# Kernel tuning notes

Hardware: AMD Instinct MI355X
Metric: run time of the kernel (lower is better)

The kernel has to match this reference:

```python
import jax, jax.numpy as jnp
import numpy as np

D_MODEL = 1024
NUM_HEADS = 16
D_K = D_MODEL // NUM_HEADS
B, S = 2, 2048
NEG = -1e9


def setup_inputs() -> dict:
    key = jax.random.key(0)
    ks = jax.random.split(key, 12)
    scale = 1.0 / np.sqrt(D_MODEL)
    inp = {
        'q': jax.random.normal(ks[0], (B, S, D_MODEL), jnp.float32),
        'k': jax.random.normal(ks[1], (B, S, D_MODEL), jnp.float32),
        'v': jax.random.normal(ks[2], (B, S, D_MODEL), jnp.float32),
        'mask': jax.random.randint(ks[3], (1, 1, S, S), 0, 2, jnp.int32),
        'wq_w': jax.random.normal(ks[4], (D_MODEL, D_MODEL), jnp.float32) * scale,
        'wq_b': jnp.zeros((D_MODEL,), jnp.float32),
        'wk_w': jax.random.normal(ks[5], (D_MODEL, D_MODEL), jnp.float32) * scale,
        'wk_b': jnp.zeros((D_MODEL,), jnp.float32),
        'wv_w': jax.random.normal(ks[6], (D_MODEL, D_MODEL), jnp.float32) * scale,
        'wv_b': jnp.zeros((D_MODEL,), jnp.float32),
        'wo_w': jax.random.normal(ks[7], (D_MODEL, D_MODEL), jnp.float32) * scale,
        'wo_b': jnp.zeros((D_MODEL,), jnp.float32),
    }
    return inp


def _split_heads(x):
    # [B,S,D] -> [B,H,S,d_k]
    b, s, _ = x.shape
    return x.reshape(b, s, NUM_HEADS, D_K).transpose(0, 2, 1, 3)


def reference(q, k, v, mask, wq_w, wq_b, wk_w, wk_b, wv_w, wv_b, wo_w, wo_b):
    # torch Linear: y = x @ W.T + b
    qh = _split_heads(q @ wq_w.T + wq_b)
    kh = _split_heads(k @ wk_w.T + wk_b)
    vh = _split_heads(v @ wv_w.T + wv_b)
    scores = jnp.einsum('bhqd,bhkd->bhqk', qh, kh) / jnp.sqrt(jnp.float32(D_K))
    scores = jnp.where(mask == 0, jnp.float32(NEG), scores)
    attn = jax.nn.softmax(scores, axis=-1)  # dropout p=0 (eval): no-op
    x = jnp.einsum('bhqk,bhkd->bhqd', attn, vh)
    x = x.transpose(0, 2, 1, 3).reshape(q.shape[0], q.shape[1], D_MODEL)
    return x @ wo_w.T + wo_b
```

## Files before the change

kernel.cpp:

```cpp
#include <hip/hip_runtime.h>
#include <hip/hip_bf16.h>
#include <stdint.h>

#define S_LEN  2048
#define DMODEL 1024
#define NHEADS 16
#define DKH    64
#define KDIM   1024

typedef __bf16 bf16x8 __attribute__((ext_vector_type(8)));
typedef float  floatx4 __attribute__((ext_vector_type(4)));
typedef unsigned short ushort8v __attribute__((ext_vector_type(8)));

__device__ inline void gll16(const __bf16* g, const __bf16* l) {
    __builtin_amdgcn_global_load_lds(
        (const __attribute__((address_space(1))) void*)g,
        (__attribute__((address_space(3))) void*)l, 16, 0, 0);
}

__global__ __launch_bounds__(256) void convert_all_kernel(
    const float* __restrict__ q, const float* __restrict__ k, const float* __restrict__ v,
    const float* __restrict__ wq, const float* __restrict__ wk, const float* __restrict__ wv,
    const float* __restrict__ wo, __bf16* __restrict__ out) {
    const size_t i8 = ((size_t)blockIdx.x * 256 + threadIdx.x) * 8;
    const float* src;
    if (i8 < 4194304u)        src = q  + i8;
    else if (i8 < 8388608u)   src = k  + (i8 - 4194304u);
    else if (i8 < 12582912u)  src = v  + (i8 - 8388608u);
    else if (i8 < 13631488u)  src = wq + (i8 - 12582912u);
    else if (i8 < 14680064u)  src = wk + (i8 - 13631488u);
    else if (i8 < 15728640u)  src = wv + (i8 - 14680064u);
    else                      src = wo + (i8 - 15728640u);
    floatx4 a = *(const floatx4*)src;
    floatx4 b = *(const floatx4*)(src + 4);
    bf16x8 r;
#pragma unroll
    for (int i = 0; i < 4; ++i) { r[i] = (__bf16)a[i]; r[i + 4] = (__bf16)b[i]; }
    *(bf16x8*)(out + i8) = r;
}

__global__ __launch_bounds__(256) void maskpack_kernel(const int* __restrict__ M,
                                                       uint64_t* __restrict__ P) {
    const size_t i = (size_t)blockIdx.x * 256 + threadIdx.x;
    uint64_t bits = __ballot(M[i] != 0);
    if ((threadIdx.x & 63) == 0) P[i >> 6] = bits;
}

__global__ __launch_bounds__(256) void qkv_gemm(
    const __bf16* __restrict__ qb, const __bf16* __restrict__ kb, const __bf16* __restrict__ vb,
    const __bf16* __restrict__ wqw, const __bf16* __restrict__ wkw, const __bf16* __restrict__ wvw,
    const float* __restrict__ biasq, const float* __restrict__ biask, const float* __restrict__ biasv,
    __bf16* __restrict__ qh, __bf16* __restrict__ kh, __bf16* __restrict__ vt) {
    __shared__ __align__(16) __bf16 As[2 * 128 * 32];
    __shared__ __align__(16) __bf16 Bs[2 * 128 * 32];

    const int lane = threadIdx.x & 63;
    const int wave = threadIdx.x >> 6;
    const int quad = lane >> 4;
    const int l15  = lane & 15;

    const int bid = blockIdx.x;
    const int job = bid >> 8;
    const int tt  = bid & 255;
    const __bf16* A; const __bf16* Bm; const float* bias; __bf16* C;
    int bx, by, MODE;
    if (job == 0)      { A = qb;  Bm = wqw; bias = biasq; C = qh; bx = tt & 7;  by = tt >> 3; MODE = 0; }
    else if (job == 1) { A = kb;  Bm = wkw; bias = biask; C = kh; bx = tt & 7;  by = tt >> 3; MODE = 0; }
    else               { A = wvw; Bm = vb;  bias = biasv; C = vt; bx = tt & 31; by = tt >> 5; MODE = 1; }

    const int m_t = by * 128, n_t = bx * 128;
    const int m0w = (wave >> 1) * 64, n0w = (wave & 1) * 64;

    const int sp = wave >> 1;
    const int sr = (wave & 1) * 64;
    const int lrow = lane >> 2;
    const int scol = ((lane & 3) ^ (lrow & 3)) * 8;

    floatx4 acc[4][4];
#pragma unroll
    for (int i = 0; i < 4; ++i)
#pragma unroll
        for (int j = 0; j < 4; ++j)
            acc[i][j] = (floatx4){0.f, 0.f, 0.f, 0.f};

    for (int kk = 0; kk < KDIM; kk += 64) {
#pragma unroll
        for (int c = 0; c < 4; ++c) {
            const int row = sr + c * 16 + lrow;
            gll16(A + (size_t)(m_t + row) * KDIM + kk + sp * 32 + scol,
                  As + (sp * 128 + sr + c * 16) * 32);
            gll16(Bm + (size_t)(n_t + row) * KDIM + kk + sp * 32 + scol,
                  Bs + (sp * 128 + sr + c * 16) * 32);
        }
        __syncthreads();
        const int cq = (quad ^ (l15 & 3)) * 8;
#pragma unroll
        for (int p = 0; p < 2; ++p) {
            bf16x8 af[4], bfr[4];
#pragma unroll
            for (int i = 0; i < 4; ++i)
                af[i] = *(const bf16x8*)(As + (p * 128 + m0w + i * 16 + l15) * 32 + cq);
#pragma unroll
            for (int j = 0; j < 4; ++j)
                bfr[j] = *(const bf16x8*)(Bs + (p * 128 + n0w + j * 16 + l15) * 32 + cq);
#pragma unroll
            for (int i = 0; i < 4; ++i)
#pragma unroll
                for (int j = 0; j < 4; ++j)
                    acc[i][j] = __builtin_amdgcn_mfma_f32_16x16x32_bf16(af[i], bfr[j], acc[i][j], 0, 0, 0);
        }
        __syncthreads();
    }

#pragma unroll
    for (int j = 0; j < 4; ++j) {
        const int n = n_t + n0w + j * 16 + l15;
        float bn = (MODE == 1) ? 0.f : bias[n];
#pragma unroll
        for (int i = 0; i < 4; ++i) {
#pragma unroll
            for (int r = 0; r < 4; ++r) {
                const int m = m_t + m0w + i * 16 + quad * 4 + r;
                float bv = (MODE == 1) ? bias[m] : bn;
                float v = acc[i][j][r] + bv;
                size_t off;
                if (MODE == 0) {
                    off = ((size_t)((m >> 11) * 16 + (n >> 6)) * 2048 + (m & 2047)) * 64 + (n & 63);
                } else {
                    off = ((size_t)((n >> 11) * 16 + (m >> 6)) * 64 + (m & 63)) * 2048 + (n & 2047);
                }
                C[off] = (__bf16)v;
            }
        }
    }
}

__global__ __launch_bounds__(256) void gemm_out(const __bf16* __restrict__ A,
                                                const __bf16* __restrict__ Bm,
                                                const float* __restrict__ bias,
                                                float* __restrict__ C) {
    __shared__ __align__(16) __bf16 As[2 * 128 * 32];
    __shared__ __align__(16) __bf16 Bs[2 * 64 * 32];

    const int lane = threadIdx.x & 63;
    const int wave = threadIdx.x >> 6;
    const int quad = lane >> 4;
    const int l15  = lane & 15;
    const int m_t = blockIdx.y * 128, n_t = blockIdx.x * 64;
    const int m0w = (wave >> 1) * 64, n0w = (wave & 1) * 32;

    const int lrow = lane >> 2;
    const int scol = ((lane & 3) ^ (lrow & 3)) * 8;

    floatx4 acc[4][2];
#pragma unroll
    for (int i = 0; i < 4; ++i)
#pragma unroll
        for (int j = 0; j < 2; ++j)
            acc[i][j] = (floatx4){0.f, 0.f, 0.f, 0.f};

    for (int kk = 0; kk < KDIM; kk += 64) {
#pragma unroll
        for (int u = 0; u < 6; ++u) {
            const int pi = wave * 6 + u;
            if (pi < 16) {
                const int panel = pi >> 3, rb = pi & 7;
                gll16(A + (size_t)(m_t + rb * 16 + lrow) * KDIM + kk + panel * 32 + scol,
                      As + (panel * 128 + rb * 16) * 32);
            } else {
                const int qi = pi - 16, panel = qi >> 2, rb = qi & 3;
                gll16(Bm + (size_t)(n_t + rb * 16 + lrow) * KDIM + kk + panel * 32 + scol,
                      Bs + (panel * 64 + rb * 16) * 32);
            }
        }
        __syncthreads();
        const int cq = (quad ^ (l15 & 3)) * 8;
#pragma unroll
        for (int p = 0; p < 2; ++p) {
            bf16x8 af[4], bfr[2];
#pragma unroll
            for (int i = 0; i < 4; ++i)
                af[i] = *(const bf16x8*)(As + (p * 128 + m0w + i * 16 + l15) * 32 + cq);
#pragma unroll
            for (int j = 0; j < 2; ++j)
                bfr[j] = *(const bf16x8*)(Bs + (p * 64 + n0w + j * 16 + l15) * 32 + cq);
#pragma unroll
            for (int i = 0; i < 4; ++i)
#pragma unroll
                for (int j = 0; j < 2; ++j)
                    acc[i][j] = __builtin_amdgcn_mfma_f32_16x16x32_bf16(af[i], bfr[j], acc[i][j], 0, 0, 0);
        }
        __syncthreads();
    }

#pragma unroll
    for (int j = 0; j < 2; ++j) {
        const int n = n_t + n0w + j * 16 + l15;
        const float bn = bias[n];
#pragma unroll
        for (int i = 0; i < 4; ++i)
#pragma unroll
            for (int r = 0; r < 4; ++r) {
                const int m = m_t + m0w + i * 16 + quad * 4 + r;
                C[(size_t)m * 1024 + n] = acc[i][j][r] + bn;
            }
    }
}

__global__ __launch_bounds__(256) void attn_kernel(const __bf16* __restrict__ Qh,
                                                   const __bf16* __restrict__ Kh,
                                                   const __bf16* __restrict__ Vt,
                                                   const uint64_t* __restrict__ PM,
                                                   __bf16* __restrict__ X) {
    __shared__ __align__(16) __bf16 Ks[2][4096];
    __shared__ __align__(16) __bf16 Vs[2][4096];

    const int lane = threadIdx.x & 63;
    const int wave = threadIdx.x >> 6;
    const int quad = lane >> 4;
    const int l15  = lane & 15;
    const int l7   = l15 & 7;

    const int bid  = blockIdx.x;
    const int xcd  = bid & 7;
    const int slot = bid >> 3;
    const int grp  = xcd * 4 + (slot >> 4);
    const int qt   = slot & 15;
    const int b = grp >> 4, h = grp & 15;
    const int q0 = qt * 128 + wave * 32;

    const __bf16* Qb = Qh + (size_t)(b * NHEADS + h) * S_LEN * DKH;
    const __bf16* Kb = Kh + (size_t)(b * NHEADS + h) * S_LEN * DKH;
    const __bf16* Vb = Vt + (size_t)(b * NHEADS + h) * DKH * S_LEN;
    const uint64_t* pr0 = PM + (size_t)(q0 + l15) * (S_LEN / 64);
    const uint64_t* pr1 = PM + (size_t)(q0 + 16 + l15) * (S_LEN / 64);

    const float cs = 0.18033688011112042f;
    const float MB = 4.0f;

    size_t offK[2], offV[2];
#pragma unroll
    for (int i = 0; i < 2; ++i) {
        const int s = wave * 128 + i * 64 + lane;
        const int r = s >> 3, cp = s & 7, c = cp ^ (r & 7);
        const int kr = (r >> 5) * 32 + ((r >> 4) & 1) * 4 + ((r >> 2) & 3) * 8 + (r & 3);
        offK[i] = (size_t)kr * DKH + c * 8;
        offV[i] = (size_t)r * S_LEN + c * 8;
    }

    bf16x8 qf[2][2];
#pragma unroll
    for (int s = 0; s < 2; ++s)
#pragma unroll
        for (int c = 0; c < 2; ++c)
            qf[s][c] = *(const bf16x8*)(Qb + (size_t)(q0 + s * 16 + l15) * DKH + c * 32 + quad * 8);

    floatx4 o[2][4];
#pragma unroll
    for (int s = 0; s < 2; ++s)
#pragma unroll
        for (int f = 0; f < 4; ++f) o[s][f] = (floatx4){0.f, 0.f, 0.f, 0.f};
    float lsum[2] = {0.f, 0.f};

    auto stage = [&](int p, int key0) {
#pragma unroll
        for (int i = 0; i < 2; ++i) {
            gll16(Kb + (size_t)key0 * DKH + offK[i], &Ks[p][(wave * 128 + i * 64) * 8]);
            gll16(Vb + key0 + offV[i],               &Vs[p][(wave * 128 + i * 64) * 8]);
        }
    };

    stage(0, 0);
    for (int kt = 0; kt < 32; ++kt) {
        const int p = kt & 1;
        __syncthreads();
        if (kt < 31) stage(p ^ 1, (kt + 1) * 64);

        const uint64_t mw0 = pr0[kt];
        const uint64_t mw1 = pr1[kt];

        bf16x8 kf[4][2];
#pragma unroll
        for (int t = 0; t < 4; ++t)
#pragma unroll
            for (int hh = 0; hh < 2; ++hh) {
                const int cp = ((hh * 4 + quad) ^ l7) * 8;
                kf[t][hh] = *(const bf16x8*)&Ks[p][(t * 16 + l15) * 64 + cp];
            }

        floatx4 st[2][4];
#pragma unroll
        for (int s = 0; s < 2; ++s)
#pragma unroll
            for (int t = 0; t < 4; ++t) {
                floatx4 z = (floatx4){0.f, 0.f, 0.f, 0.f};
                z = __builtin_amdgcn_mfma_f32_16x16x32_bf16(kf[t][0], qf[s][0], z, 0, 0, 0);
                z = __builtin_amdgcn_mfma_f32_16x16x32_bf16(kf[t][1], qf[s][1], z, 0, 0, 0);
                st[s][t] = z;
            }

        bf16x8 pw[2][2];
#pragma unroll
        for (int s = 0; s < 2; ++s) {
            const uint64_t mw = s ? mw1 : mw0;
#pragma unroll
            for (int w = 0; w < 2; ++w) {
                bf16x8 pb;
#pragma unroll
                for (int half = 0; half < 2; ++half) {
                    const int t = w * 2 + half;
                    const int sh = w * 32 + half * 4 + quad * 8;
#pragma unroll
                    for (int r = 0; r < 4; ++r) {
                        float e = exp2f(fmaf(st[s][t][r], cs, -MB));
                        e = ((mw >> (sh + r)) & 1u) ? e : 0.f;
                        lsum[s] += e;
                        pb[half * 4 + r] = (__bf16)e;
                    }
                }
                pw[s][w] = pb;
            }
        }

#pragma unroll
        for (int w = 0; w < 2; ++w) {
            const int cp = ((w * 4 + quad) ^ l7) * 8;
#pragma unroll
            for (int f = 0; f < 4; ++f) {
                bf16x8 vf = *(const bf16x8*)&Vs[p][(f * 16 + l15) * 64 + cp];
                o[0][f] = __builtin_amdgcn_mfma_f32_16x16x32_bf16(vf, pw[0][w], o[0][f], 0, 0, 0);
                o[1][f] = __builtin_amdgcn_mfma_f32_16x16x32_bf16(vf, pw[1][w], o[1][f], 0, 0, 0);
            }
        }
    }

    float inv[2];
#pragma unroll
    for (int s = 0; s < 2; ++s) {
        float t = lsum[s];
        t += __shfl_xor(t, 16);
        t += __shfl_xor(t, 32);
        inv[s] = (t > 0.f) ? (1.f / t) : 0.f;
    }

    __syncthreads();
    unsigned short* xw = (unsigned short*)&Ks[0][0] + wave * (16 * 80);
#pragma unroll
    for (int s = 0; s < 2; ++s) {
#pragma unroll
        for (int f = 0; f < 4; ++f)
#pragma unroll
            for (int r = 0; r < 4; ++r) {
                __bf16 bv = (__bf16)(o[s][f][r] * inv[s]);
                xw[l15 * 80 + f * 16 + quad * 4 + r] = __builtin_bit_cast(unsigned short, bv);
            }
#pragma unroll
        for (int it = 0; it < 2; ++it) {
            const int ql = it * 8 + (lane >> 3);
            const int dseg = (lane & 7) * 8;
            ushort8v vv = *(const ushort8v*)&xw[ql * 80 + dseg];
            unsigned short* dst = (unsigned short*)X +
                (size_t)(b * S_LEN + q0 + s * 16 + ql) * DMODEL + h * DKH + dseg;
            *(ushort8v*)dst = vv;
        }
    }
}

extern "C" void kernel_launch(void* const* d_in, const int* in_sizes, int n_in,
                              void* d_out, int out_size, void* d_ws, size_t ws_size,
                              hipStream_t stream) {
    const float* q   = (const float*)d_in[0];
    const float* k   = (const float*)d_in[1];
    const float* v   = (const float*)d_in[2];
    const int*   msk = (const int*)d_in[3];
    const float* wq  = (const float*)d_in[4];
    const float* wqb = (const float*)d_in[5];
    const float* wk  = (const float*)d_in[6];
    const float* wkb = (const float*)d_in[7];
    const float* wv  = (const float*)d_in[8];
    const float* wvb = (const float*)d_in[9];
    const float* wo  = (const float*)d_in[10];
    const float* wob = (const float*)d_in[11];

    char* ws = (char*)d_ws;
    __bf16*   qh   = (__bf16*)(ws);
    __bf16*   kh   = (__bf16*)(ws + 8388608);
    __bf16*   vt   = (__bf16*)(ws + 16777216);
    uint64_t* pm   = (uint64_t*)(ws + 25165824);
    __bf16*   cb   = (__bf16*)(ws + 25690112);
    __bf16*   qb   = cb;
    __bf16*   kb   = cb + 4194304;
    __bf16*   vb   = cb + 8388608;
    __bf16*   wqbf = cb + 12582912;
    __bf16*   wkbf = cb + 13631488;
    __bf16*   wvbf = cb + 14680064;
    __bf16*   wobf = cb + 15728640;
    __bf16*   xa   = qb;

    convert_all_kernel<<<8192, 256, 0, stream>>>(q, k, v, wq, wk, wv, wo, cb);
    maskpack_kernel<<<16384, 256, 0, stream>>>(msk, pm);
    qkv_gemm<<<768, 256, 0, stream>>>(qb, kb, vb, wqbf, wkbf, wvbf, wqb, wkb, wvb, qh, kh, vt);
    attn_kernel<<<512, 256, 0, stream>>>(qh, kh, vt, pm, xa);
    gemm_out<<<dim3(16, 32), 256, 0, stream>>>(xa, wobf, wob, (float*)d_out);
}
```

Measured before the change: 296.4 us.

## Halve attention query tile per wave, double grid, compute row sums via MFMA

The attention kernel now gives each wave 16 query rows instead of 32, so each block covers 64 queries and the grid doubles to 1024 blocks with a launch-bounds occupancy hint of 4. The softmax denominator is accumulated with an extra MFMA against a ones vector instead of per-lane adds and shuffles. The code also uses a hardware exp2 builtin, applies the mask with a sign-bit AND, and prefetches the mask word one iteration ahead. The aim is more waves in flight and fewer VALU instructions, at the cost of reloading K/V tiles from LDS for half as many queries per block, which roughly doubles K/V traffic.

```diff
diff --git a/kernel.cpp b/kernel.cpp
--- a/kernel.cpp
+++ b/kernel.cpp
@@ -16,6 +16,14 @@
     __builtin_amdgcn_global_load_lds(
         (const __attribute__((address_space(1))) void*)g,
         (__attribute__((address_space(3))) void*)l, 16, 0, 0);
+}
+
+__device__ inline float fast_exp2(float x) {
+#if __has_builtin(__builtin_amdgcn_exp2f)
+    return __builtin_amdgcn_exp2f(x);
+#else
+    return exp2f(x);
+#endif
 }
 
 __global__ __launch_bounds__(256) void convert_all_kernel(
@@ -207,11 +215,11 @@
     }
 }
 
-__global__ __launch_bounds__(256) void attn_kernel(const __bf16* __restrict__ Qh,
-                                                   const __bf16* __restrict__ Kh,
-                                                   const __bf16* __restrict__ Vt,
-                                                   const uint64_t* __restrict__ PM,
-                                                   __bf16* __restrict__ X) {
+__global__ __launch_bounds__(256, 4) void attn_kernel(const __bf16* __restrict__ Qh,
+                                                      const __bf16* __restrict__ Kh,
+                                                      const __bf16* __restrict__ Vt,
+                                                      const uint64_t* __restrict__ PM,
+                                                      __bf16* __restrict__ X) {
     __shared__ __align__(16) __bf16 Ks[2][4096];
     __shared__ __align__(16) __bf16 Vs[2][4096];
 
@@ -224,16 +232,15 @@
     const int bid  = blockIdx.x;
     const int xcd  = bid & 7;
     const int slot = bid >> 3;
-    const int grp  = xcd * 4 + (slot >> 4);
-    const int qt   = slot & 15;
+    const int grp  = xcd * 4 + (slot >> 5);
+    const int qt   = slot & 31;
     const int b = grp >> 4, h = grp & 15;
-    const int q0 = qt * 128 + wave * 32;
+    const int q0 = qt * 64 + wave * 16;
 
     const __bf16* Qb = Qh + (size_t)(b * NHEADS + h) * S_LEN * DKH;
     const __bf16* Kb = Kh + (size_t)(b * NHEADS + h) * S_LEN * DKH;
     const __bf16* Vb = Vt + (size_t)(b * NHEADS + h) * DKH * S_LEN;
-    const uint64_t* pr0 = PM + (size_t)(q0 + l15) * (S_LEN / 64);
-    const uint64_t* pr1 = PM + (size_t)(q0 + 16 + l15) * (S_LEN / 64);
+    const uint64_t* pr = PM + (size_t)(q0 + l15) * (S_LEN / 64);
 
     const float cs = 0.18033688011112042f;
     const float MB = 4.0f;
@@ -248,19 +255,19 @@
         offV[i] = (size_t)r * S_LEN + c * 8;
     }
 
-    bf16x8 qf[2][2];
-#pragma unroll
-    for (int s = 0; s < 2; ++s)
-#pragma unroll
-        for (int c = 0; c < 2; ++c)
-            qf[s][c] = *(const bf16x8*)(Qb + (size_t)(q0 + s * 16 + l15) * DKH + c * 32 + quad * 8);
-
-    floatx4 o[2][4];
-#pragma unroll
-    for (int s = 0; s < 2; ++s)
-#pragma unroll
-        for (int f = 0; f < 4; ++f) o[s][f] = (floatx4){0.f, 0.f, 0.f, 0.f};
-    float lsum[2] = {0.f, 0.f};
+    bf16x8 qf[2];
+#pragma unroll
+    for (int c = 0; c < 2; ++c)
+        qf[c] = *(const bf16x8*)(Qb + (size_t)(q0 + l15) * DKH + c * 32 + quad * 8);
+
+    bf16x8 ones;
+#pragma unroll
+    for (int i = 0; i < 8; ++i) ones[i] = (__bf16)1.0f;
+
+    floatx4 o[4], osum;
+#pragma unroll
+    for (int f = 0; f < 4; ++f) o[f] = (floatx4){0.f, 0.f, 0.f, 0.f};
+    osum = (floatx4){0.f, 0.f, 0.f, 0.f};
 
     auto stage = [&](int p, int key0) {
 #pragma unroll
@@ -271,13 +278,13 @@
     };
 
     stage(0, 0);
+    uint2 mwc = *(const uint2*)(pr);
     for (int kt = 0; kt < 32; ++kt) {
         const int p = kt & 1;
         __syncthreads();
         if (kt < 31) stage(p ^ 1, (kt + 1) * 64);
-
-        const uint64_t mw0 = pr0[kt];
-        const uint64_t mw1 = pr1[kt];
+        const uint2 mw = mwc;
+        if (kt < 31) mwc = *(const uint2*)(pr + kt + 1);
 
         bf16x8 kf[4][2];
 #pragma unroll
@@ -288,38 +295,33 @@
                 kf[t][hh] = *(const bf16x8*)&Ks[p][(t * 16 + l15) * 64 + cp];
             }
 
-        floatx4 st[2][4];
-#pragma unroll
-        for (int s = 0; s < 2; ++s)
-#pragma unroll
-            for (int t = 0; t < 4; ++t) {
-                floatx4 z = (floatx4){0.f, 0.f, 0.f, 0.f};
-                z = __builtin_amdgcn_mfma_f32_16x16x32_bf16(kf[t][0], qf[s][0], z, 0, 0, 0);
-                z = __builtin_amdgcn_mfma_f32_16x16x32_bf16(kf[t][1], qf[s][1], z, 0, 0, 0);
-                st[s][t] = z;
-            }
-
-        bf16x8 pw[2][2];
-#pragma unroll
-        for (int s = 0; s < 2; ++s) {
-            const uint64_t mw = s ? mw1 : mw0;
-#pragma unroll
-            for (int w = 0; w < 2; ++w) {
-                bf16x8 pb;
-#pragma unroll
-                for (int half = 0; half < 2; ++half) {
-                    const int t = w * 2 + half;
-                    const int sh = w * 32 + half * 4 + quad * 8;
-#pragma unroll
-                    for (int r = 0; r < 4; ++r) {
-                        float e = exp2f(fmaf(st[s][t][r], cs, -MB));
-                        e = ((mw >> (sh + r)) & 1u) ? e : 0.f;
-                        lsum[s] += e;
-                        pb[half * 4 + r] = (__bf16)e;
-                    }
+        floatx4 st[4];
+#pragma unroll
+        for (int t = 0; t < 4; ++t) {
+            floatx4 z = (floatx4){0.f, 0.f, 0.f, 0.f};
+            z = __builtin_amdgcn_mfma_f32_16x16x32_bf16(kf[t][0], qf[0], z, 0, 0, 0);
+            z = __builtin_amdgcn_mfma_f32_16x16x32_bf16(kf[t][1], qf[1], z, 0, 0, 0);
+            st[t] = z;
+        }
+
+        bf16x8 pw[2];
+#pragma unroll
+        for (int w = 0; w < 2; ++w) {
+            const uint32_t byte = (w ? mw.y : mw.x) >> (quad * 8);
+            bf16x8 pb;
+#pragma unroll
+            for (int half = 0; half < 2; ++half) {
+                const int t = w * 2 + half;
+#pragma unroll
+                for (int r = 0; r < 4; ++r) {
+                    const int idx = half * 4 + r;
+                    float e = fast_exp2(fmaf(st[t][r], cs, -MB));
+                    const int sgn = ((int)(byte << (31 - idx))) >> 31;
+                    e = __builtin_bit_cast(float, __builtin_bit_cast(int, e) & sgn);
+                    pb[half * 4 + r] = (__bf16)e;
                 }
-                pw[s][w] = pb;
-            }
+            }
+            pw[w] = pb;
         }
 
 #pragma unroll
@@ -328,41 +330,32 @@
 #pragma unroll
             for (int f = 0; f < 4; ++f) {
                 bf16x8 vf = *(const bf16x8*)&Vs[p][(f * 16 + l15) * 64 + cp];
-                o[0][f] = __builtin_amdgcn_mfma_f32_16x16x32_bf16(vf, pw[0][w], o[0][f], 0, 0, 0);
-                o[1][f] = __builtin_amdgcn_mfma_f32_16x16x32_bf16(vf, pw[1][w], o[1][f], 0, 0, 0);
-            }
-        }
-    }
-
-    float inv[2];
-#pragma unroll
-    for (int s = 0; s < 2; ++s) {
-        float t = lsum[s];
-        t += __shfl_xor(t, 16);
-        t += __shfl_xor(t, 32);
-        inv[s] = (t > 0.f) ? (1.f / t) : 0.f;
-    }
+                o[f] = __builtin_amdgcn_mfma_f32_16x16x32_bf16(vf, pw[w], o[f], 0, 0, 0);
+            }
+            osum = __builtin_amdgcn_mfma_f32_16x16x32_bf16(ones, pw[w], osum, 0, 0, 0);
+        }
+    }
+
+    const float lsum = osum[0];
+    const float inv = (lsum > 0.f) ? (1.f / lsum) : 0.f;
 
     __syncthreads();
     unsigned short* xw = (unsigned short*)&Ks[0][0] + wave * (16 * 80);
 #pragma unroll
-    for (int s = 0; s < 2; ++s) {
-#pragma unroll
-        for (int f = 0; f < 4; ++f)
-#pragma unroll
-            for (int r = 0; r < 4; ++r) {
-                __bf16 bv = (__bf16)(o[s][f][r] * inv[s]);
-                xw[l15 * 80 + f * 16 + quad * 4 + r] = __builtin_bit_cast(unsigned short, bv);
-            }
-#pragma unroll
-        for (int it = 0; it < 2; ++it) {
-            const int ql = it * 8 + (lane >> 3);
-            const int dseg = (lane & 7) * 8;
-            ushort8v vv = *(const ushort8v*)&xw[ql * 80 + dseg];
-            unsigned short* dst = (unsigned short*)X +
-                (size_t)(b * S_LEN + q0 + s * 16 + ql) * DMODEL + h * DKH + dseg;
-            *(ushort8v*)dst = vv;
-        }
+    for (int f = 0; f < 4; ++f)
+#pragma unroll
+        for (int r = 0; r < 4; ++r) {
+            __bf16 bv = (__bf16)(o[f][r] * inv);
+            xw[l15 * 80 + f * 16 + quad * 4 + r] = __builtin_bit_cast(unsigned short, bv);
+        }
+#pragma unroll
+    for (int it = 0; it < 2; ++it) {
+        const int ql = it * 8 + (lane >> 3);
+        const int dseg = (lane & 7) * 8;
+        ushort8v vv = *(const ushort8v*)&xw[ql * 80 + dseg];
+        unsigned short* dst = (unsigned short*)X +
+            (size_t)(b * S_LEN + q0 + ql) * DMODEL + h * DKH + dseg;
+        *(ushort8v*)dst = vv;
     }
 }
 
@@ -400,6 +393,6 @@
     convert_all_kernel<<<8192, 256, 0, stream>>>(q, k, v, wq, wk, wv, wo, cb);
     maskpack_kernel<<<16384, 256, 0, stream>>>(msk, pm);
     qkv_gemm<<<768, 256, 0, stream>>>(qb, kb, vb, wqbf, wkbf, wvbf, wqb, wkb, wvb, qh, kh, vt);
-    attn_kernel<<<512, 256, 0, stream>>>(qh, kh, vt, pm, xa);
+    attn_kernel<<<1024, 256, 0, stream>>>(qh, kh, vt, pm, xa);
     gemm_out<<<dim3(16, 32), 256, 0, stream>>>(xa, wobf, wob, (float*)d_out);
 }
```

After: 274.8 us. 1.08x faster.
